# Optimization experiments

Hardware: AMD Instinct MI355X
Metric: run time of the kernel (lower is better)

The kernel has to match this reference:

```python
import jax, jax.numpy as jnp
import numpy as np

SCALE = 1.0
DENSE = 4
ITERS = 5


def setup_inputs() -> dict:
    key = jax.random.key(0)
    k1, k2, k3 = jax.random.split(key, 3)
    data = jax.random.normal(k1, (8, 32, 512, 512), dtype=jnp.float32)
    # nonnegative marginal attention maps (strictly positive to keep sums safe)
    attx = jax.random.uniform(k2, (8, 512, 1), dtype=jnp.float32, minval=0.01, maxval=1.0)
    atty = jax.random.uniform(k3, (8, 512, 1), dtype=jnp.float32, minval=0.01, maxval=1.0)
    return {"data": data, "attx": attx, "atty": atty}


def _axis_coords(att, out_size):
    """Iterative clipped inverse-CDF sampling coords (AttSamplerGrid math).

    att: (N, S) nonnegative marginal attention. Returns coords in [-1, 1], (N, out_size).
    """
    N, S = att.shape
    att = att / jnp.sum(att, axis=1, keepdims=True) * out_size  # sum == out_size
    thr = DENSE * out_size / S  # each input cell maps to at most `dense` output pixels
    for _ in range(ITERS):
        att = jnp.minimum(att, thr)
        # redistribute clipped mass uniformly so the sum returns to out_size
        att = att + (out_size - jnp.sum(att, axis=1, keepdims=True)) / S
    csum = jnp.cumsum(att, axis=1)                      # (N, S) monotone CDF * out_size
    step = csum[:, -1:] / out_size                      # (N, 1), ~1.0
    tgt = step * jnp.arange(1, out_size + 1, dtype=att.dtype)[None, :]  # (N, out)
    # first index j with csum[j] >= target  (inverse CDF)
    j = jax.vmap(lambda c, t: jnp.searchsorted(c, t, side='left'))(csum, tgt)
    j = jnp.clip(j, 0, S - 1)
    right = jnp.take_along_axis(csum, j, axis=1)
    left = jnp.where(j > 0, jnp.take_along_axis(csum, jnp.maximum(j - 1, 0), axis=1), 0.0)
    frac = jnp.clip((tgt - left) / jnp.maximum(right - left, 1e-8), 0.0, 1.0)
    return (j.astype(att.dtype) + frac) / S * 2.0 - 1.0


def _lerp_axis(x, coord, axis):
    """1-D linear interpolation of x along `axis` at normalized coords in [-1,1].

    x: (N, C, H, W); coord: (N, L). align_corners=True mapping, coords stay in-range
    so zero-padding never triggers (bilinear grid_sample is separable for this grid).
    """
    size = x.shape[axis]
    p = (coord + 1.0) * 0.5 * (size - 1)
    p0f = jnp.floor(p)
    w = p - p0f                                         # (N, L)
    i0 = jnp.clip(p0f.astype(jnp.int32), 0, size - 1)
    i1 = jnp.clip(i0 + 1, 0, size - 1)
    shp = [coord.shape[0], 1, 1, 1]
    shp[axis] = coord.shape[1]
    i0 = i0.reshape(shp)
    i1 = i1.reshape(shp)
    w = w.reshape(shp)
    x0 = jnp.take_along_axis(x, i0, axis=axis)
    x1 = jnp.take_along_axis(x, i1, axis=axis)
    return x0 * (1.0 - w) + x1 * w


def reference(data, attx, atty):
    N, C, H, W = data.shape
    out_h = int(round(H * SCALE))
    out_w = int(round(W * SCALE))
    gx = _axis_coords(attx[..., 0], out_w)   # (N, out_w) x-coords (width)
    gy = _axis_coords(atty[..., 0], out_h)   # (N, out_h) y-coords (height)
    cols = _lerp_axis(data, gx, axis=3)      # (N, C, H, out_w)
    out = _lerp_axis(cols, gy, axis=2)       # (N, C, out_h, out_w)
    return out
```

## Files before the change

kernel.cpp:

```cpp
#include <hip/hip_runtime.h>

#define S    512
#define OUT  512
#define NB   8
#define CB   32
#define WPB  2
#define NSPP 64
#define NBLK (NB * CB * (NSPP / WPB))

__global__ __launch_bounds__(64) void coords_kernel(
    const float* __restrict__ attx, const float* __restrict__ atty,
    int2* __restrict__ coords,
    int* __restrict__ bnd)
{
  __shared__ double sc[S];
  __shared__ int pr[S];
  const int lane = threadIdx.x;
  const int n    = blockIdx.x & 7;
  const int axis = blockIdx.x >> 3;
  const float* att = (axis == 0 ? attx : atty) + n * S;

  double a[8];
#pragma unroll
  for (int k = 0; k < 8; ++k) a[k] = (double)att[lane * 8 + k];

  double tot = 0.0;
#pragma unroll
  for (int k = 0; k < 8; ++k) tot += a[k];
#pragma unroll
  for (int off = 32; off > 0; off >>= 1) tot += __shfl_xor(tot, off);

#pragma unroll
  for (int k = 0; k < 8; ++k) a[k] = a[k] / tot * (double)OUT;
  const double thr = (double)(4 * OUT) / (double)S;

  for (int it = 0; it < 5; ++it) {
    double s = 0.0;
#pragma unroll
    for (int k = 0; k < 8; ++k) { a[k] = a[k] < thr ? a[k] : thr; s += a[k]; }
#pragma unroll
    for (int off = 32; off > 0; off >>= 1) s += __shfl_xor(s, off);
    const double corr = ((double)OUT - s) / (double)S;
#pragma unroll
    for (int k = 0; k < 8; ++k) a[k] += corr;
  }

  double p[8]; double run = 0.0;
#pragma unroll
  for (int k = 0; k < 8; ++k) { run += a[k]; p[k] = run; }
  double v = run;
#pragma unroll
  for (int off = 1; off < 64; off <<= 1) {
    double t = __shfl_up(v, off);
    if (lane >= off) v += t;
  }
  const double excl = v - run;
#pragma unroll
  for (int k = 0; k < 8; ++k) sc[lane * 8 + k] = excl + p[k];
  __syncthreads();

  const double step = sc[S - 1] / (double)OUT;

  int i0s[8];
#pragma unroll
  for (int k = 0; k < 8; ++k) {
    const int ox = lane * 8 + k;
    const double tgt = step * (double)(ox + 1);

    int lo = 0, hi = S;
    while (lo < hi) {
      int mid = (lo + hi) >> 1;
      if (sc[mid] < tgt) lo = mid + 1; else hi = mid;
    }
    int j = lo < S - 1 ? lo : S - 1;

    double right = sc[j];
    double left  = (j > 0) ? sc[j - 1] : 0.0;
    double denom = right - left;
    if (denom < 1e-8) denom = 1e-8;
    double frac = (tgt - left) / denom;
    frac = frac < 0.0 ? 0.0 : (frac > 1.0 ? 1.0 : frac);

    double pp  = ((double)j + frac) / (double)S * (double)(S - 1);
    double p0f = floor(pp);
    double w   = pp - p0f;
    int i0 = (int)p0f;
    i0 = i0 < 0 ? 0 : (i0 > S - 1 ? S - 1 : i0);
    i0s[k] = i0;

    coords[(axis * NB + n) * S + ox] = make_int2(i0, __float_as_int((float)w));
  }

  if (axis == 1) {
    const int fromPrev = __shfl_up(i0s[7], 1);
    int prevv = (lane == 0) ? (i0s[0] - 2) : fromPrev;
    int cinc[8]; int runc = 0;
#pragma unroll
    for (int k = 0; k < 8; ++k) {
      const int d = i0s[k] - prevv;
      const int c = 1 + (d <= 0 ? 0 : (d == 1 ? 1 : 2));
      runc += c; cinc[k] = runc; prevv = i0s[k];
    }
    int vv = runc;
#pragma unroll
    for (int off = 1; off < 64; off <<= 1) {
      const int t = __shfl_up(vv, off);
      if (lane >= off) vv += t;
    }
    const int exclc = vv - runc;
#pragma unroll
    for (int k = 0; k < 8; ++k) pr[lane * 8 + k] = exclc + cinc[k];
    __syncthreads();

    const int Ctot = pr[S - 1];
    const int tgt = (int)(((long long)lane * Ctot) / NSPP);
    int lo = 0, hi = S;
    while (lo < hi) {
      const int mid = (lo + hi) >> 1;
      if (pr[mid] <= tgt) lo = mid + 1; else hi = mid;
    }
    bnd[n * (NSPP + 1) + lane] = lo;
    if (lane == 63) bnd[n * (NSPP + 1) + NSPP] = S;
  }
}

__global__ __launch_bounds__(128) void sample_kernel(
    const float* __restrict__ data, const int2* __restrict__ coords,
    const int* __restrict__ bnd, float* __restrict__ out)
{
  __shared__ float bufA_[WPB][S + 1];
  __shared__ float bufB_[WPB][S + 1];

  int b = (int)blockIdx.x;
  b = (b & 7) * (NBLK / 8) + (b >> 3);
  const int plane = b >> 5;
  const int bip   = b & 31;
  const int n     = plane >> 5;

  const int tid  = threadIdx.x;
  const int wv   = tid >> 6;
  const int lane = tid & 63;
  const int s    = bip * WPB + wv;
  const int oy0   = bnd[n * (NSPP + 1) + s];
  const int oyend = bnd[n * (NSPP + 1) + s + 1];

  const float* __restrict__ pl = data + (size_t)plane * (S * S);
  float* __restrict__       po = out  + (size_t)plane * (S * S);

  int   ix[8];
  float wx[8];
#pragma unroll
  for (int k = 0; k < 8; ++k) {
    const int2 cx = coords[n * S + lane + 64 * k];
    ix[k] = cx.x;
    wx[k] = __int_as_float(cx.y);
  }

  float* bufA = bufA_[wv];
  float* bufB = bufB_[wv];
  const int2* __restrict__ cyp = coords + (NB + n) * S;

  float CxA[8], CxB[8];
  int curA = -1000;

  for (int oy = oy0; oy < oyend; ++oy) {
    const int2 cy = cyp[oy];
    const int   a  = cy.x;
    const float wy = __int_as_float(cy.y);

    if (a != curA) {
      const int rowB = (a + 1 < S) ? a + 1 : S - 1;
      if (a == curA + 1) {
#pragma unroll
        for (int k = 0; k < 8; ++k) CxA[k] = CxB[k];
        const float4* RB = (const float4*)(pl + (size_t)rowB * S);
        const float4 p0 = RB[lane];
        const float4 p1 = RB[lane + 64];
        ((float4*)bufB)[lane]      = p0;
        ((float4*)bufB)[lane + 64] = p1;
        if (lane == 63) bufB[S] = p1.w;
#pragma unroll
        for (int k = 0; k < 8; ++k) {
          const float x0 = bufB[ix[k]];
          const float x1 = bufB[ix[k] + 1];
          CxB[k] = x0 + wx[k] * (x1 - x0);
        }
      } else {
        const float4* RA = (const float4*)(pl + (size_t)a    * S);
        const float4* RB = (const float4*)(pl + (size_t)rowB * S);
        const float4 q0 = RA[lane];
        const float4 q1 = RA[lane + 64];
        const float4 p0 = RB[lane];
        const float4 p1 = RB[lane + 64];
        ((float4*)bufA)[lane]      = q0;
        ((float4*)bufA)[lane + 64] = q1;
        ((float4*)bufB)[lane]      = p0;
        ((float4*)bufB)[lane + 64] = p1;
        if (lane == 63) { bufA[S] = q1.w; bufB[S] = p1.w; }
#pragma unroll
        for (int k = 0; k < 8; ++k) {
          const float x0 = bufA[ix[k]];
          const float x1 = bufA[ix[k] + 1];
          CxA[k] = x0 + wx[k] * (x1 - x0);
        }
#pragma unroll
        for (int k = 0; k < 8; ++k) {
          const float x0 = bufB[ix[k]];
          const float x1 = bufB[ix[k] + 1];
          CxB[k] = x0 + wx[k] * (x1 - x0);
        }
      }
      curA = a;
    }

    float* orow = po + (size_t)oy * OUT;
#pragma unroll
    for (int k = 0; k < 8; ++k)
      __builtin_nontemporal_store(CxA[k] + wy * (CxB[k] - CxA[k]),
                                  orow + lane + 64 * k);
  }
}

extern "C" void kernel_launch(void* const* d_in, const int* in_sizes, int n_in,
                              void* d_out, int out_size, void* d_ws, size_t ws_size,
                              hipStream_t stream) {
  const float* data = (const float*)d_in[0];
  const float* attx = (const float*)d_in[1];
  const float* atty = (const float*)d_in[2];
  float* out = (float*)d_out;

  int2* coords = (int2*)d_ws;
  int*  bnd    = (int*)((char*)d_ws + 2 * NB * S * sizeof(int2));

  coords_kernel<<<16, 64, 0, stream>>>(attx, atty, coords, bnd);

  sample_kernel<<<NBLK, 128, 0, stream>>>(data, coords, bnd, out);
}
```

Baseline: 99.40 us.

## Software-pipeline row loads by prefetching next output row's source rows into registers

Each wave now loads the global source rows needed by the next output row into registers while it computes and stores the current row, then commits them to LDS at the start of the next iteration. This hides global-load latency behind the horizontal interpolation and store work instead of stalling on each new row. It also adds an early exit for empty ranges. In exchange it needs more registers for the prefetched float4s and adds branching on the transition type.

```diff
diff --git a/kernel.cpp b/kernel.cpp
--- a/kernel.cpp
+++ b/kernel.cpp
@@ -143,6 +143,7 @@
   const int s    = bip * WPB + wv;
   const int oy0   = bnd[n * (NSPP + 1) + s];
   const int oyend = bnd[n * (NSPP + 1) + s + 1];
+  if (oy0 >= oyend) return;
 
   const float* __restrict__ pl = data + (size_t)plane * (S * S);
   float* __restrict__       po = out  + (size_t)plane * (S * S);
@@ -161,63 +162,90 @@
   const int2* __restrict__ cyp = coords + (NB + n) * S;
 
   float CxA[8], CxB[8];
-  int curA = -1000;
+  float4 qA0, qA1, qB0, qB1;
+
+  int prevA;
+  int tcur;
+  float wyc;
+  {
+    const int2 c = cyp[oy0];
+    const int a = c.x;
+    wyc = __int_as_float(c.y);
+    const int rb = (a + 1 < S) ? a + 1 : S - 1;
+    const float4* RA = (const float4*)(pl + (size_t)a  * S);
+    const float4* RB = (const float4*)(pl + (size_t)rb * S);
+    qA0 = RA[lane]; qA1 = RA[lane + 64];
+    qB0 = RB[lane]; qB1 = RB[lane + 64];
+    tcur = 2;
+    prevA = a;
+  }
 
   for (int oy = oy0; oy < oyend; ++oy) {
-    const int2 cy = cyp[oy];
-    const int   a  = cy.x;
-    const float wy = __int_as_float(cy.y);
-
-    if (a != curA) {
-      const int rowB = (a + 1 < S) ? a + 1 : S - 1;
-      if (a == curA + 1) {
-#pragma unroll
-        for (int k = 0; k < 8; ++k) CxA[k] = CxB[k];
-        const float4* RB = (const float4*)(pl + (size_t)rowB * S);
-        const float4 p0 = RB[lane];
-        const float4 p1 = RB[lane + 64];
-        ((float4*)bufB)[lane]      = p0;
-        ((float4*)bufB)[lane + 64] = p1;
-        if (lane == 63) bufB[S] = p1.w;
-#pragma unroll
-        for (int k = 0; k < 8; ++k) {
-          const float x0 = bufB[ix[k]];
-          const float x1 = bufB[ix[k] + 1];
-          CxB[k] = x0 + wx[k] * (x1 - x0);
+    if (tcur == 2) {
+      ((float4*)bufA)[lane]      = qA0;
+      ((float4*)bufA)[lane + 64] = qA1;
+      ((float4*)bufB)[lane]      = qB0;
+      ((float4*)bufB)[lane + 64] = qB1;
+      if (lane == 63) { bufA[S] = qA1.w; bufB[S] = qB1.w; }
+    } else if (tcur == 1) {
+      ((float4*)bufB)[lane]      = qB0;
+      ((float4*)bufB)[lane + 64] = qB1;
+      if (lane == 63) bufB[S] = qB1.w;
+    }
+
+    int tnext = 0;
+    float wyn = 0.0f;
+    if (oy + 1 < oyend) {
+      const int2 c = cyp[oy + 1];
+      const int a = c.x;
+      wyn = __int_as_float(c.y);
+      if (a != prevA) {
+        const int rb = (a + 1 < S) ? a + 1 : S - 1;
+        const float4* RB = (const float4*)(pl + (size_t)rb * S);
+        qB0 = RB[lane]; qB1 = RB[lane + 64];
+        if (a == prevA + 1) {
+          tnext = 1;
+        } else {
+          const float4* RA = (const float4*)(pl + (size_t)a * S);
+          qA0 = RA[lane]; qA1 = RA[lane + 64];
+          tnext = 2;
         }
-      } else {
-        const float4* RA = (const float4*)(pl + (size_t)a    * S);
-        const float4* RB = (const float4*)(pl + (size_t)rowB * S);
-        const float4 q0 = RA[lane];
-        const float4 q1 = RA[lane + 64];
-        const float4 p0 = RB[lane];
-        const float4 p1 = RB[lane + 64];
-        ((float4*)bufA)[lane]      = q0;
-        ((float4*)bufA)[lane + 64] = q1;
-        ((float4*)bufB)[lane]      = p0;
-        ((float4*)bufB)[lane + 64] = p1;
-        if (lane == 63) { bufA[S] = q1.w; bufB[S] = p1.w; }
-#pragma unroll
-        for (int k = 0; k < 8; ++k) {
-          const float x0 = bufA[ix[k]];
-          const float x1 = bufA[ix[k] + 1];
-          CxA[k] = x0 + wx[k] * (x1 - x0);
-        }
-#pragma unroll
-        for (int k = 0; k < 8; ++k) {
-          const float x0 = bufB[ix[k]];
-          const float x1 = bufB[ix[k] + 1];
-          CxB[k] = x0 + wx[k] * (x1 - x0);
-        }
-      }
-      curA = a;
+        prevA = a;
+      }
+    }
+
+    if (tcur == 2) {
+#pragma unroll
+      for (int k = 0; k < 8; ++k) {
+        const float x0 = bufA[ix[k]];
+        const float x1 = bufA[ix[k] + 1];
+        CxA[k] = x0 + wx[k] * (x1 - x0);
+      }
+#pragma unroll
+      for (int k = 0; k < 8; ++k) {
+        const float x0 = bufB[ix[k]];
+        const float x1 = bufB[ix[k] + 1];
+        CxB[k] = x0 + wx[k] * (x1 - x0);
+      }
+    } else if (tcur == 1) {
+#pragma unroll
+      for (int k = 0; k < 8; ++k) CxA[k] = CxB[k];
+#pragma unroll
+      for (int k = 0; k < 8; ++k) {
+        const float x0 = bufB[ix[k]];
+        const float x1 = bufB[ix[k] + 1];
+        CxB[k] = x0 + wx[k] * (x1 - x0);
+      }
     }
 
     float* orow = po + (size_t)oy * OUT;
 #pragma unroll
     for (int k = 0; k < 8; ++k)
-      __builtin_nontemporal_store(CxA[k] + wy * (CxB[k] - CxA[k]),
+      __builtin_nontemporal_store(CxA[k] + wyc * (CxB[k] - CxA[k]),
                                   orow + lane + 64 * k);
+
+    tcur = tnext;
+    wyc  = wyn;
   }
 }
 
```

New measurement: 138.4 us. 39.3% more time.
